# Optimization experiments

Hardware: AMD Instinct MI355X
Metric: run time of the kernel (lower is better)

The kernel has to match this reference:

```python
import jax, jax.numpy as jnp
import numpy as np

EPS = 1e-9

def setup_inputs() -> dict:
    key = jax.random.key(0)
    k1, k2, k3 = jax.random.split(key, 3)
    B, S, H = 16, 4096, 768
    input_data = jax.random.normal(k1, (B, S, H), dtype=jnp.float32)
    # nn.Linear(hidden_size, 1): weight [1, H], bias [1]; store as [H, 1] for matmul
    W = jax.random.normal(k2, (H, 1), dtype=jnp.float32) * (1.0 / np.sqrt(H))
    b = jax.random.normal(k3, (1,), dtype=jnp.float32) * 0.01
    return {"input_data": input_data, "W": W, "b": b}

def _exclusive_cumsum(t):
    # exclusive prefix sum along seq axis (axis=1): out[:, i] = sum_{j < i} t[:, j]
    c = jnp.cumsum(t, axis=1)
    return jnp.pad(c, ((0, 0), (1, 0), (0, 0)))[:, :-1]

def reference(input_data, W, b):
    # attention score a_j = exp(w . x_j + b), shape [B, S, 1]
    a = jnp.exp(input_data @ W + b)
    # Original: out[b, i] = (sum_{j < i} a_j * x_j) / (sum_{j < i} a_j + 1e-9)
    # (triu(ones, 1).T is the strict lower-triangular causal mask).
    # Equivalent O(S*H) form via exclusive prefix sums:
    num = _exclusive_cumsum(a * input_data)          # [B, S, H]
    den = _exclusive_cumsum(a) + EPS                 # [B, S, 1]
    return num / den
```

## Files before the change

kernel.cpp:

```cpp
#include <hip/hip_runtime.h>
#include <math.h>

#define NB 16
#define NS 4096
#define NH 768
#define NC 64
#define CHUNK 64

static constexpr float kEps = 1e-9f;

__global__ __launch_bounds__(256) void la_k1(
    const float* __restrict__ x, const float* __restrict__ Wp,
    const float* __restrict__ bp,
    float* __restrict__ a, float* __restrict__ partial,
    float* __restrict__ asum)
{
  const int blk  = blockIdx.x;
  const int b    = blk >> 6;
  const int c    = blk & 63;
  const int t    = threadIdx.x;
  const int w    = t >> 6;
  const int lane = t & 63;
  const float bias = bp[0];

  const float4* W4 = reinterpret_cast<const float4*>(Wp);
  const float4 w0 = W4[lane];
  const float4 w1 = W4[64 + lane];
  const float4 w2 = W4[128 + lane];

  float4 acc0 = {0.f,0.f,0.f,0.f};
  float4 acc1 = {0.f,0.f,0.f,0.f};
  float4 acc2 = {0.f,0.f,0.f,0.f};
  float wsum = 0.f;
  float areg = 0.f;

  const int row0 = c * CHUNK + w * 16;
  const float* xb = x + (size_t)(b * NS + row0) * NH;

  #pragma unroll 2
  for (int r = 0; r < 16; ++r) {
    const float4* X4 = reinterpret_cast<const float4*>(xb + (size_t)r * NH);
    const float4 x0 = X4[lane];
    const float4 x1 = X4[64 + lane];
    const float4 x2 = X4[128 + lane];
    float dot = x0.x*w0.x + x0.y*w0.y + x0.z*w0.z + x0.w*w0.w
              + x1.x*w1.x + x1.y*w1.y + x1.z*w1.z + x1.w*w1.w
              + x2.x*w2.x + x2.y*w2.y + x2.z*w2.z + x2.w*w2.w;
    #pragma unroll
    for (int off = 1; off < 64; off <<= 1) dot += __shfl_xor(dot, off);
    const float aj = expf(dot + bias);
    if (lane == r) areg = aj;
    wsum += aj;
    acc0.x += aj*x0.x; acc0.y += aj*x0.y; acc0.z += aj*x0.z; acc0.w += aj*x0.w;
    acc1.x += aj*x1.x; acc1.y += aj*x1.y; acc1.z += aj*x1.z; acc1.w += aj*x1.w;
    acc2.x += aj*x2.x; acc2.y += aj*x2.y; acc2.z += aj*x2.z; acc2.w += aj*x2.w;
  }
  if (lane < 16) a[(size_t)b * NS + row0 + lane] = areg;

  __shared__ float lacc[4 * NH];
  __shared__ float lsum[4];
  float4* l4 = reinterpret_cast<float4*>(lacc) + (size_t)w * (NH / 4);
  l4[lane]       = acc0;
  l4[64 + lane]  = acc1;
  l4[128 + lane] = acc2;
  if (lane == 0) lsum[w] = wsum;
  __syncthreads();

  float* pd = partial + (size_t)blk * NH;
  #pragma unroll
  for (int k = 0; k < 3; ++k) {
    const int h = t + k * 256;
    pd[h] = lacc[h] + lacc[NH + h] + lacc[2 * NH + h] + lacc[3 * NH + h];
  }
  if (t == 0) asum[blk] = lsum[0] + lsum[1] + lsum[2] + lsum[3];
}

__global__ __launch_bounds__(1024) void la_k2(float* __restrict__ partial)
{
  const int hg = blockIdx.x;
  const int b  = blockIdx.y;
  const int t  = threadIdx.x;
  const int c  = t >> 4;
  const int hh = t & 15;
  const int h  = hg * 16 + hh;
  const size_t idx = (size_t)(b * NC + c) * NH + h;

  const float v = partial[idx];
  __shared__ float lds[NC][16];
  lds[c][hh] = v;
  __syncthreads();
  #pragma unroll
  for (int off = 1; off < 64; off <<= 1) {
    const float n = (c >= off) ? lds[c - off][hh] : 0.f;
    __syncthreads();
    lds[c][hh] += n;
    __syncthreads();
  }
  partial[idx] = lds[c][hh] - v;
}

__global__ __launch_bounds__(192) void la_k3(
    const float* __restrict__ x, const float* __restrict__ a,
    const float* __restrict__ offs ,
    const float* __restrict__ asum,
    float* __restrict__ out)
{
  const int blk = blockIdx.x;
  const int b   = blk >> 6;
  const int c   = blk & 63;
  const int t   = threadIdx.x;
  const int h4  = t * 4;

  __shared__ float la[CHUNK];
  __shared__ float s_aofs;
  if (t < CHUNK) la[t] = a[(size_t)b * NS + c * CHUNK + t];
  if (t < 64) {
    float av = (t < c) ? asum[b * NC + t] : 0.f;
    #pragma unroll
    for (int off = 1; off < 64; off <<= 1) av += __shfl_xor(av, off);
    if (t == 0) s_aofs = av;
  }

  float4 acc = *reinterpret_cast<const float4*>(offs + (size_t)blk * NH + h4);
  __syncthreads();
  const float aofs = s_aofs;

  const size_t base = ((size_t)b * NS + (size_t)c * CHUNK) * NH + h4;
  const float* xb = x + base;
  float*       ob = out + base;

  float runa = 0.f;
  float4 xv = *reinterpret_cast<const float4*>(xb);
  #pragma unroll 2
  for (int j = 0; j < CHUNK; ++j) {
    float4 xn = {0.f,0.f,0.f,0.f};
    if (j + 1 < CHUNK)
      xn = *reinterpret_cast<const float4*>(xb + (size_t)(j + 1) * NH);
    const float aj  = la[j];
    const float den = aofs + runa + kEps;
    const float inv = __builtin_amdgcn_rcpf(den);
    float4 o;
    o.x = acc.x * inv; o.y = acc.y * inv; o.z = acc.z * inv; o.w = acc.w * inv;
    *reinterpret_cast<float4*>(ob + (size_t)j * NH) = o;
    acc.x += aj * xv.x; acc.y += aj * xv.y; acc.z += aj * xv.z; acc.w += aj * xv.w;
    runa += aj;
    xv = xn;
  }
}

extern "C" void kernel_launch(void* const* d_in, const int* in_sizes, int n_in,
                              void* d_out, int out_size, void* d_ws, size_t ws_size,
                              hipStream_t stream) {
  const float* x  = (const float*)d_in[0];
  const float* Wp = (const float*)d_in[1];
  const float* bp = (const float*)d_in[2];
  float* out = (float*)d_out;

  char* ws = (char*)d_ws;
  float* a       = (float*)(ws);
  float* partial = (float*)(ws + 262144);
  float* asum    = (float*)(ws + 262144 + 3145728);

  la_k1<<<NB * NC, 256, 0, stream>>>(x, Wp, bp, a, partial, asum);
  la_k2<<<dim3(NH / 16, NB), 1024, 0, stream>>>(partial);
  la_k3<<<NB * NC, 192, 0, stream>>>(x, a, partial, asum, out);
}
```

Before: 384.3 us.

## Fuse three kernels into one single-pass scan with inter-block flags

Replaces the three-kernel pipeline (chunk reduce, cross-chunk scan, output pass) with one kernel. Each block publishes its chunk aggregate, raises a release flag, waits for earlier chunks' flags, then sums their aggregates serially to get its exclusive prefix. The block also keeps its x tile hot and writes the outputs, removing the separate scan kernel and part of the global traffic. In exchange it depends on blocks of the same batch row being co-resident to avoid deadlock. Each block also does an O(c) serial read of prior aggregates, and the output pass re-reads x from global memory.

Measured after the change: 836.8 us. +117.7%, slower.

```diff
diff --git a/kernel.cpp b/kernel.cpp
--- a/kernel.cpp
+++ b/kernel.cpp
@@ -6,14 +6,17 @@
 #define NH 768
 #define NC 64
 #define CHUNK 64
+#define NBLK (NB * NC)
 
 static constexpr float kEps = 1e-9f;
 
-__global__ __launch_bounds__(256) void la_k1(
+__global__ __launch_bounds__(256, 4) void la_fused(
     const float* __restrict__ x, const float* __restrict__ Wp,
     const float* __restrict__ bp,
-    float* __restrict__ a, float* __restrict__ partial,
-    float* __restrict__ asum)
+    float* __restrict__ agg,
+    float* __restrict__ agg_a,
+    unsigned int* __restrict__ flag,
+    float* __restrict__ out)
 {
   const int blk  = blockIdx.x;
   const int b    = blk >> 6;
@@ -22,6 +25,12 @@
   const int w    = t >> 6;
   const int lane = t & 63;
   const float bias = bp[0];
+
+  __shared__ float lacc[4][NH];
+  __shared__ float la[CHUNK];
+  __shared__ float lsum[4];
+  __shared__ float cex[NH];
+  __shared__ float cex_a;
 
   const float4* W4 = reinterpret_cast<const float4*>(Wp);
   const float4 w0 = W4[lane];
@@ -48,103 +57,106 @@
               + x2.x*w2.x + x2.y*w2.y + x2.z*w2.z + x2.w*w2.w;
     #pragma unroll
     for (int off = 1; off < 64; off <<= 1) dot += __shfl_xor(dot, off);
-    const float aj = expf(dot + bias);
+    const float aj = __expf(dot + bias);
     if (lane == r) areg = aj;
     wsum += aj;
     acc0.x += aj*x0.x; acc0.y += aj*x0.y; acc0.z += aj*x0.z; acc0.w += aj*x0.w;
     acc1.x += aj*x1.x; acc1.y += aj*x1.y; acc1.z += aj*x1.z; acc1.w += aj*x1.w;
     acc2.x += aj*x2.x; acc2.y += aj*x2.y; acc2.z += aj*x2.z; acc2.w += aj*x2.w;
   }
-  if (lane < 16) a[(size_t)b * NS + row0 + lane] = areg;
-
-  __shared__ float lacc[4 * NH];
-  __shared__ float lsum[4];
-  float4* l4 = reinterpret_cast<float4*>(lacc) + (size_t)w * (NH / 4);
-  l4[lane]       = acc0;
-  l4[64 + lane]  = acc1;
-  l4[128 + lane] = acc2;
+  if (lane < 16) la[w * 16 + lane] = areg;
+  {
+    float4* l4 = reinterpret_cast<float4*>(lacc[w]);
+    l4[lane]       = acc0;
+    l4[64 + lane]  = acc1;
+    l4[128 + lane] = acc2;
+  }
   if (lane == 0) lsum[w] = wsum;
   __syncthreads();
 
-  float* pd = partial + (size_t)blk * NH;
-  #pragma unroll
-  for (int k = 0; k < 3; ++k) {
-    const int h = t + k * 256;
-    pd[h] = lacc[h] + lacc[NH + h] + lacc[2 * NH + h] + lacc[3 * NH + h];
+  {
+    float* ag = agg + (size_t)blk * NH;
+    #pragma unroll
+    for (int k = 0; k < 3; ++k) {
+      const int h = t + k * 256;
+      ag[h] = lacc[0][h] + lacc[1][h] + lacc[2][h] + lacc[3][h];
+    }
+    if (t == 0) agg_a[blk] = lsum[0] + lsum[1] + lsum[2] + lsum[3];
   }
-  if (t == 0) asum[blk] = lsum[0] + lsum[1] + lsum[2] + lsum[3];
-}
+  __threadfence();
+  __syncthreads();
+  if (t == 0)
+    __hip_atomic_store(&flag[blk], 1u, __ATOMIC_RELEASE, __HIP_MEMORY_SCOPE_AGENT);
 
-__global__ __launch_bounds__(1024) void la_k2(float* __restrict__ partial)
-{
-  const int hg = blockIdx.x;
-  const int b  = blockIdx.y;
-  const int t  = threadIdx.x;
-  const int c  = t >> 4;
-  const int hh = t & 15;
-  const int h  = hg * 16 + hh;
-  const size_t idx = (size_t)(b * NC + c) * NH + h;
+  if (t < c) {
+    while (__hip_atomic_load(&flag[b * NC + t], __ATOMIC_ACQUIRE,
+                             __HIP_MEMORY_SCOPE_AGENT) == 0u) {
+      __builtin_amdgcn_s_sleep(1);
+    }
+  }
+  __syncthreads();
+  __threadfence();
 
-  const float v = partial[idx];
-  __shared__ float lds[NC][16];
-  lds[c][hh] = v;
-  __syncthreads();
-  #pragma unroll
-  for (int off = 1; off < 64; off <<= 1) {
-    const float n = (c >= off) ? lds[c - off][hh] : 0.f;
-    __syncthreads();
-    lds[c][hh] += n;
-    __syncthreads();
+  {
+    float e0 = 0.f, e1 = 0.f, e2 = 0.f;
+    for (int cc = 0; cc < c; ++cc) {
+      const float* ap = agg + (size_t)(b * NC + cc) * NH;
+      e0 += ap[t];
+      e1 += ap[t + 256];
+      e2 += ap[t + 512];
+    }
+    cex[t]       = e0;
+    cex[t + 256] = e1;
+    cex[t + 512] = e2;
   }
-  partial[idx] = lds[c][hh] - v;
-}
-
-__global__ __launch_bounds__(192) void la_k3(
-    const float* __restrict__ x, const float* __restrict__ a,
-    const float* __restrict__ offs ,
-    const float* __restrict__ asum,
-    float* __restrict__ out)
-{
-  const int blk = blockIdx.x;
-  const int b   = blk >> 6;
-  const int c   = blk & 63;
-  const int t   = threadIdx.x;
-  const int h4  = t * 4;
-
-  __shared__ float la[CHUNK];
-  __shared__ float s_aofs;
-  if (t < CHUNK) la[t] = a[(size_t)b * NS + c * CHUNK + t];
-  if (t < 64) {
-    float av = (t < c) ? asum[b * NC + t] : 0.f;
+  if (w == 0) {
+    float av = (lane < c) ? agg_a[b * NC + lane] : 0.f;
     #pragma unroll
     for (int off = 1; off < 64; off <<= 1) av += __shfl_xor(av, off);
-    if (t == 0) s_aofs = av;
+    if (lane == 0) cex_a = av;
   }
+  __syncthreads();
 
-  float4 acc = *reinterpret_cast<const float4*>(offs + (size_t)blk * NH + h4);
-  __syncthreads();
-  const float aofs = s_aofs;
+  float4 s0, s1, s2;
+  {
+    const float4* cx4 = reinterpret_cast<const float4*>(cex);
+    s0 = cx4[lane]; s1 = cx4[64 + lane]; s2 = cx4[128 + lane];
+    for (int w2 = 0; w2 < w; ++w2) {
+      const float4* l4c = reinterpret_cast<const float4*>(lacc[w2]);
+      const float4 a0 = l4c[lane], a1 = l4c[64 + lane], a2 = l4c[128 + lane];
+      s0.x += a0.x; s0.y += a0.y; s0.z += a0.z; s0.w += a0.w;
+      s1.x += a1.x; s1.y += a1.y; s1.z += a1.z; s1.w += a1.w;
+      s2.x += a2.x; s2.y += a2.y; s2.z += a2.z; s2.w += a2.w;
+    }
+  }
+  float dena = cex_a;
+  for (int w2 = 0; w2 < w; ++w2) dena += lsum[w2];
 
-  const size_t base = ((size_t)b * NS + (size_t)c * CHUNK) * NH + h4;
-  const float* xb = x + base;
-  float*       ob = out + base;
+  float* ob = out + (size_t)(b * NS + row0) * NH;
+  const float4* Xp = reinterpret_cast<const float4*>(xb);
+  float4 p0 = Xp[lane], p1 = Xp[64 + lane], p2 = Xp[128 + lane];
 
-  float runa = 0.f;
-  float4 xv = *reinterpret_cast<const float4*>(xb);
-  #pragma unroll 2
-  for (int j = 0; j < CHUNK; ++j) {
-    float4 xn = {0.f,0.f,0.f,0.f};
-    if (j + 1 < CHUNK)
-      xn = *reinterpret_cast<const float4*>(xb + (size_t)(j + 1) * NH);
-    const float aj  = la[j];
-    const float den = aofs + runa + kEps;
-    const float inv = __builtin_amdgcn_rcpf(den);
-    float4 o;
-    o.x = acc.x * inv; o.y = acc.y * inv; o.z = acc.z * inv; o.w = acc.w * inv;
-    *reinterpret_cast<float4*>(ob + (size_t)j * NH) = o;
-    acc.x += aj * xv.x; acc.y += aj * xv.y; acc.z += aj * xv.z; acc.w += aj * xv.w;
-    runa += aj;
-    xv = xn;
+  for (int r = 0; r < 16; ++r) {
+    float4 n0, n1, n2;
+    if (r + 1 < 16) {
+      const float4* Xn = reinterpret_cast<const float4*>(xb + (size_t)(r + 1) * NH);
+      n0 = Xn[lane]; n1 = Xn[64 + lane]; n2 = Xn[128 + lane];
+    }
+    const float aj  = la[w * 16 + r];
+    const float inv = __builtin_amdgcn_rcpf(dena + kEps);
+    float4* O4 = reinterpret_cast<float4*>(ob + (size_t)r * NH);
+    float4 o0, o1, o2;
+    o0.x = s0.x*inv; o0.y = s0.y*inv; o0.z = s0.z*inv; o0.w = s0.w*inv;
+    o1.x = s1.x*inv; o1.y = s1.y*inv; o1.z = s1.z*inv; o1.w = s1.w*inv;
+    o2.x = s2.x*inv; o2.y = s2.y*inv; o2.z = s2.z*inv; o2.w = s2.w*inv;
+    O4[lane]       = o0;
+    O4[64 + lane]  = o1;
+    O4[128 + lane] = o2;
+    s0.x += aj*p0.x; s0.y += aj*p0.y; s0.z += aj*p0.z; s0.w += aj*p0.w;
+    s1.x += aj*p1.x; s1.y += aj*p1.y; s1.z += aj*p1.z; s1.w += aj*p1.w;
+    s2.x += aj*p2.x; s2.y += aj*p2.y; s2.z += aj*p2.z; s2.w += aj*p2.w;
+    dena += aj;
+    if (r + 1 < 16) { p0 = n0; p1 = n1; p2 = n2; }
   }
 }
 
@@ -157,11 +169,11 @@
   float* out = (float*)d_out;
 
   char* ws = (char*)d_ws;
-  float* a       = (float*)(ws);
-  float* partial = (float*)(ws + 262144);
-  float* asum    = (float*)(ws + 262144 + 3145728);
+  float*        agg   = (float*)(ws);
+  float*        agg_a = (float*)(ws + 3145728);
+  unsigned int* flag  = (unsigned int*)(ws + 3145728 + 4096);
 
-  la_k1<<<NB * NC, 256, 0, stream>>>(x, Wp, bp, a, partial, asum);
-  la_k2<<<dim3(NH / 16, NB), 1024, 0, stream>>>(partial);
-  la_k3<<<NB * NC, 192, 0, stream>>>(x, a, partial, asum, out);
+  hipMemsetAsync(flag, 0, NBLK * sizeof(unsigned int), stream);
+
+  la_fused<<<NBLK, 256, 0, stream>>>(x, Wp, bp, agg, agg_a, flag, out);
 }
```
